# Optimization experiments

Measured on AMD Instinct MI355X. Metric: run time of the kernel, lower is better.

Reference implementation:

```python
import jax, jax.numpy as jnp
import numpy as np

LAMBDA_FGW = 0.5
TAU_KL = 0.1
N_OUTER = 5
N_SINKHORN = 10
DIM = 512


def _pdist(a, b):
    # sqrt(clamp(||a-b||^2, 1e-6)) computed via expansion (avoids BxKxMxD temp)
    n2 = ((a * a).sum(-1)[:, :, None] + (b * b).sum(-1)[:, None, :]
          - 2.0 * jnp.einsum('bkd,bmd->bkm', a, b))
    return jnp.sqrt(jnp.clip(n2, 1e-6, None))


def setup_inputs() -> dict:
    key = jax.random.key(0)
    ks = jax.random.split(key, 10)
    B, K, M, D = 256, 128, 128, DIM
    inp = {
        'sq': jax.random.normal(ks[0], (B, K, D), jnp.float32),
        'sr': jax.random.normal(ks[1], (B, M, D), jnp.float32),
        'mask_q': jax.random.uniform(ks[2], (B, K), jnp.float32),
        'mask_r': jax.random.uniform(ks[3], (B, M), jnp.float32),
        'centroids_q': jax.random.normal(ks[4], (B, K, D), jnp.float32),
        'centroids_r': jax.random.normal(ks[5], (B, M, D), jnp.float32),
        'W1': jax.random.normal(ks[6], (D, D), jnp.float32) * 0.02,
        'b1': jnp.zeros((D,), jnp.float32),
        'W2': jax.random.normal(ks[7], (D, D), jnp.float32) * 0.02,
        'b2': jnp.zeros((D,), jnp.float32),
        'log_eps': jnp.asarray(np.log(0.05), jnp.float32),
    }
    return inp


def reference(sq, sr, mask_q, mask_r, centroids_q, centroids_r, W1, b1, W2, b2, log_eps):
    proj = lambda x: jax.nn.relu(x @ W1 + b1) @ W2 + b2
    pq, pr = proj(sq), proj(sr)
    C = _pdist(pq, pr)                      # [B,K,M]
    Sq = _pdist(centroids_q, centroids_q)   # [B,K,K]
    Sr = _pdist(centroids_r, centroids_r)   # [B,M,M]

    mu = mask_q / (mask_q.sum(-1, keepdims=True) + 1e-8)  # [B,K]
    nu = mask_r / (mask_r.sum(-1, keepdims=True) + 1e-8)  # [B,M]
    T = mu[:, :, None] * nu[:, None, :]

    eps = jnp.clip(jnp.exp(log_eps), 0.01, 0.5)
    rho = TAU_KL / (TAU_KL + eps)
    log_mu = jnp.log(jnp.clip(mu, 1e-8, None))
    log_nu = jnp.log(jnp.clip(nu, 1e-8, None))
    Sq2, Sr2 = Sq * Sq, Sr * Sr

    C_fgw = C
    for _ in range(N_OUTER):
        t1 = jnp.einsum('bkl,bl->bk', Sq2, T.sum(2))[:, :, None]
        t2 = jnp.einsum('bm,bmn->bn', T.sum(1), Sr2)[:, None, :]
        L_gw = t1 + t2 - 2.0 * jnp.einsum('bkl,blm->bkm', Sq, jnp.einsum('blm,bmn->bln', T, Sr))
        C_fgw = (1.0 - LAMBDA_FGW) * C + LAMBDA_FGW * L_gw
        log_K = -C_fgw / eps
        log_u = jnp.zeros_like(mu)
        log_v = jnp.zeros_like(nu)
        for _ in range(N_SINKHORN):
            log_u = rho * (log_mu - jax.nn.logsumexp(log_K + log_v[:, None, :], axis=2))
            log_v = rho * (log_nu - jax.nn.logsumexp(log_K + log_u[:, :, None], axis=1))
        T = jnp.exp(log_u[:, :, None] + log_K + log_v[:, None, :])

    cost = (T * C_fgw).sum((-1, -2))
    similarity = jax.nn.sigmoid(-cost)
    return similarity, T, C, cost
```

## Files before the change

kernel.cpp:

```cpp
#include <hip/hip_runtime.h>
#include <math.h>

typedef unsigned short u16;
typedef __attribute__((ext_vector_type(4))) float f32x4;
typedef __attribute__((ext_vector_type(8))) short bf16x8;
typedef __attribute__((ext_vector_type(4))) unsigned short u16x4;
typedef __attribute__((ext_vector_type(8))) unsigned short u16x8;

#define DEVI static __device__ __forceinline__

DEVI float b2f(u16 u){ union{float f; unsigned i;} v; v.i = ((unsigned)u)<<16; return v.f; }
DEVI u16 f2b(float f){ union{float f; unsigned i;} v; v.f=f;
  unsigned r = v.i + 0x7fffu + ((v.i>>16)&1u); return (u16)(r>>16); }

DEVI void gload_lds16(const void* g, void* l){
  __builtin_amdgcn_global_load_lds((const __attribute__((address_space(1))) void*)g,
                                   (__attribute__((address_space(3))) void*)l, 16, 0, 0);
}

DEVI f32x4 vmax4(f32x4 a, f32x4 b){
  f32x4 r; r[0]=fmaxf(a[0],b[0]); r[1]=fmaxf(a[1],b[1]);
  r[2]=fmaxf(a[2],b[2]); r[3]=fmaxf(a[3],b[3]); return r;
}

__global__ void prepw_k(const float* __restrict__ W, u16* __restrict__ Wt){
  int id = blockIdx.x*256 + threadIdx.x;
  int k = id>>9, c = id&511;
  Wt[c*512 + k] = f2b(W[id]);
}

__global__ void cvt_k(const float* __restrict__ src, u16* __restrict__ dst,
                      float* __restrict__ norms, int nrows){
  int gw = (int)((blockIdx.x*blockDim.x + threadIdx.x)>>6);
  int lane = threadIdx.x & 63;
  if (gw >= nrows) return;
  const float* s = src + (size_t)gw*512;
  u16* d = dst + (size_t)gw*512;
  float acc = 0.f;
  #pragma unroll
  for (int q=0;q<2;q++){
    f32x4 v = *(const f32x4*)(s + q*256 + lane*4);
    u16x4 u;
    #pragma unroll
    for (int e=0;e<4;e++){
      u16 b = f2b(v[e]); u[e] = b;
      float fv = b2f(b); acc += fv*fv;
    }
    *(u16x4*)(d + q*256 + lane*4) = u;
  }
  if (norms != nullptr){
    #pragma unroll
    for (int off=1;off<64;off<<=1) acc += __shfl_xor(acc, off);
    if (lane==0) norms[gw] = acc;
  }
}

template<int ACT, int NORM>
__global__ __launch_bounds__(256) void gemm_k(const u16* __restrict__ X,
    const u16* __restrict__ Wt, const float* __restrict__ bias, u16* __restrict__ OUT,
    float* __restrict__ NP){
  __shared__ __align__(16) u16 sA[128*64];
  __shared__ __align__(16) u16 sB[128*64];
  const int tid = threadIdx.x, wave = tid>>6, lane = tid&63;
  const int bid = (blockIdx.x&7)*256 + (blockIdx.x>>3);
  const int rblk = bid>>2, cb = (bid&3)<<7;
  const u16* Xb = X + (size_t)rblk*(128*512);
  const u16* Wb = Wt + (size_t)cb*512;
  const int lrow = lane&15, lg = lane>>4, wr = wave>>1, wc = wave&1;
  f32x4 acc[4][4] = {};
  for (int s=0;s<8;s++){
    const int k0 = s<<6;
    #pragma unroll
    for (int q=0;q<4;q++){
      const int i = (wave<<2)+q;
      const int row = (i<<3) + (lane>>3);
      const int cd = (lane&7) ^ (row&7);
      gload_lds16(Xb + row*512 + k0 + (cd<<3), sA + i*512);
      gload_lds16(Wb + row*512 + k0 + (cd<<3), sB + i*512);
    }
    __syncthreads();
    #pragma unroll
    for (int kh=0;kh<2;kh++){
      bf16x8 a_[4], b_[4];
      #pragma unroll
      for (int i=0;i<4;i++){
        const int ra = (wr<<6)+(i<<4)+lrow;
        a_[i] = *(const bf16x8*)(sA + ra*64 + ((((kh<<2)+lg)^(ra&7))<<3));
        const int rb = (wc<<6)+(i<<4)+lrow;
        b_[i] = *(const bf16x8*)(sB + rb*64 + ((((kh<<2)+lg)^(rb&7))<<3));
      }
      #pragma unroll
      for (int i=0;i<4;i++)
        #pragma unroll
        for (int j=0;j<4;j++)
          acc[i][j] = __builtin_amdgcn_mfma_f32_16x16x32_bf16(a_[i], b_[j], acc[i][j], 0,0,0);
    }
    __syncthreads();
  }
  float nacc[4][4];
  if (NORM){
    #pragma unroll
    for (int i=0;i<4;i++)
      #pragma unroll
      for (int r=0;r<4;r++) nacc[i][r]=0.f;
  }
  #pragma unroll
  for (int j=0;j<4;j++){
    const int col = cb + (wc<<6) + (j<<4) + lrow;
    const float bv = bias[col];
    #pragma unroll
    for (int i=0;i<4;i++){
      const int row0 = (rblk<<7) + (wr<<6) + (i<<4) + (lg<<2);
      #pragma unroll
      for (int r=0;r<4;r++){
        float v = acc[i][j][r] + bv;
        if (ACT) v = fmaxf(v, 0.f);
        u16 pb = f2b(v);
        OUT[(size_t)(row0+r)*512 + col] = pb;
        if (NORM){ float fv = b2f(pb); nacc[i][r] += fv*fv; }
      }
    }
  }
  if (NORM){
    #pragma unroll
    for (int i=0;i<4;i++)
      #pragma unroll
      for (int r=0;r<4;r++){
        float v = nacc[i][r];
        v += __shfl_xor(v,1); v += __shfl_xor(v,2);
        v += __shfl_xor(v,4); v += __shfl_xor(v,8);
        if (lrow==0)
          atomicAdd(NP + (rblk<<7) + (wr<<6) + (i<<4) + (lg<<2) + r, v);
      }
  }
}

template<int MODE>
__global__ __launch_bounds__(256) void pdist_k(const u16* __restrict__ Xa,
    const u16* __restrict__ Xb2, const float* __restrict__ na, const float* __restrict__ nb,
    float* __restrict__ OUT, char* __restrict__ SHL){
  __shared__ __align__(16) u16 sA[128*64];
  __shared__ __align__(16) u16 sB[128*64];
  const int tid = threadIdx.x, wave = tid>>6, lane = tid&63;
  const int b = blockIdx.x;
  const u16* Ab = Xa + (size_t)b*(128*512);
  const u16* Bb = Xb2 + (size_t)b*(128*512);
  const int lrow = lane&15, lg = lane>>4, wr = wave>>1, wc = wave&1;
  f32x4 acc[4][4] = {};
  for (int s=0;s<8;s++){
    const int k0 = s<<6;
    #pragma unroll
    for (int q=0;q<4;q++){
      const int i = (wave<<2)+q;
      const int row = (i<<3) + (lane>>3);
      const int cd = (lane&7) ^ (row&7);
      gload_lds16(Ab + row*512 + k0 + (cd<<3), sA + i*512);
      gload_lds16(Bb + row*512 + k0 + (cd<<3), sB + i*512);
    }
    __syncthreads();
    #pragma unroll
    for (int kh=0;kh<2;kh++){
      bf16x8 a_[4], b_[4];
      #pragma unroll
      for (int i=0;i<4;i++){
        const int ra = (wr<<6)+(i<<4)+lrow;
        a_[i] = *(const bf16x8*)(sA + ra*64 + ((((kh<<2)+lg)^(ra&7))<<3));
        const int rb = (wc<<6)+(i<<4)+lrow;
        b_[i] = *(const bf16x8*)(sB + rb*64 + ((((kh<<2)+lg)^(rb&7))<<3));
      }
      #pragma unroll
      for (int i=0;i<4;i++)
        #pragma unroll
        for (int j=0;j<4;j++)
          acc[i][j] = __builtin_amdgcn_mfma_f32_16x16x32_bf16(a_[i], b_[j], acc[i][j], 0,0,0);
    }
    __syncthreads();
  }
  #pragma unroll
  for (int j=0;j<4;j++){
    const int col = (wc<<6)+(j<<4)+lrow;
    const float nbv = nb[b*128+col];
    #pragma unroll
    for (int i=0;i<4;i++){
      const int row0 = (wr<<6)+(i<<4)+(lg<<2);
      float sv[4];
      #pragma unroll
      for (int r=0;r<4;r++){
        float n2 = na[b*128+row0+r] + nbv - 2.0f*acc[i][j][r];
        sv[r] = sqrtf(fmaxf(n2, 1e-6f));
      }
      if (MODE==0){
        #pragma unroll
        for (int r=0;r<4;r++)
          OUT[(size_t)b*16384 + (size_t)(row0+r)*128 + col] = sv[r];
      } else {
        u16x4 hi4, lo4;
        #pragma unroll
        for (int r=0;r<4;r++){
          u16 h = f2b(sv[r]); hi4[r] = h;
          lo4[r] = f2b(sv[r] - b2f(h));
        }
        const int sa = col*256 + ((((row0>>3)^col)&15)<<4) + ((row0&7)<<1);
        char* base = SHL + (size_t)b*65536;
        *(u16x4*)(base + sa) = hi4;
        *(u16x4*)(base + 32768 + sa) = lo4;
      }
    }
  }
}

__global__ void prep_k(const float* __restrict__ mask_q, const float* __restrict__ mask_r,
                       float* __restrict__ lmu2, float* __restrict__ lnu2,
                       float* __restrict__ mu, float* __restrict__ nu){
  int b = blockIdx.x, t = threadIdx.x;
  __shared__ float red[4];
  float mq = mask_q[b*128+t], mr = mask_r[b*128+t];
  float s1 = mq, s2 = mr;
  #pragma unroll
  for (int off=1;off<64;off<<=1){ s1 += __shfl_xor(s1,off); s2 += __shfl_xor(s2,off); }
  if ((t&63)==0){ red[t>>6] = s1; red[2+(t>>6)] = s2; }
  __syncthreads();
  float sumq = red[0]+red[1], sumr = red[2]+red[3];
  float muv = mq/(sumq+1e-8f), nuv = mr/(sumr+1e-8f);
  lmu2[b*128+t] = __log2f(fmaxf(muv,1e-8f));
  lnu2[b*128+t] = __log2f(fmaxf(nuv,1e-8f));
  mu[b*128+t] = muv;
  nu[b*128+t] = nuv;
}

__global__ __launch_bounds__(512,1) void fgw_loop_k(
    const char* __restrict__ SQHL, const char* __restrict__ SRHL,
    const float* __restrict__ C_g,
    const float* __restrict__ MU, const float* __restrict__ NU,
    const float* __restrict__ LMU2, const float* __restrict__ LNU2,
    const float* __restrict__ log_eps,
    float* __restrict__ T_out, float* __restrict__ cost_out, float* __restrict__ sim_out)
{
  __shared__ __align__(16) char bufT[65536];
  __shared__ __align__(16) char bufS[65536];
  __shared__ __align__(16) float avs[128], bvs[128], t1s[128], t2s[128];
  __shared__ __align__(16) float lus[128], lvs[128];
  __shared__ float redc[8];

  const int b = blockIdx.x, tid = threadIdx.x;
  const int w = tid>>6, lane = tid&63, l15 = lane&15, lg = lane>>4;
  const char* SqHLb = SQHL + (size_t)b*65536;
  const char* SrHLb = SRHL + (size_t)b*65536;
  const float* Cb   = C_g + (size_t)b*16384;
  const float* MUb  = MU + b*128;
  const float* NUb  = NU + b*128;

  float eps = __expf(log_eps[0]); eps = fminf(fmaxf(eps,0.01f),0.5f);
  const float rho = 0.1f/(0.1f+eps);
  const float hscale = 0.5f*1.4426950408889634f/eps;

  const int kR = 16*w + l15;
  const int n0 = 16*w + 4*lg;
  const float lmu2R = LMU2[b*128+kR];
  const float lnu2C = LNU2[b*128+kR];

  const int rowA256 = (16*w + l15)*256;
  const int glo2 = lg ^ (l15 & 3);
  const int ghi2 = l15 & 12;
  const int wtail = l15*256 + ((((2*w + (lg>>1)) ^ l15)&15)<<4) + ((lg&1)<<3);

  f32x4 Cf2[8];
  #pragma unroll
  for (int kt=0;kt<8;kt++)
    Cf2[kt] = -hscale * (*(const f32x4*)(Cb + (size_t)(16*kt+l15)*128 + n0));

  f32x4 lkR[8], lkC[8];
  float luR = 0.f, lvC = 0.f;

  for (int outer=0; outer<5; outer++){
    #pragma unroll
    for (int r2=0;r2<8;r2++)
      gload_lds16(SrHLb + r2*8192 + tid*16, bufS + r2*8192 + tid*16);
    {
      f32x4 avp = {0.f,0.f,0.f,0.f};
      float bvp = 0.f;
      #pragma unroll
      for (int q=0;q<8;q++){
        f32x4 TR, TC;
        if (outer==0){
          const f32x4 nu4 = *(const f32x4*)(NUb + 16*q + 4*lg);
          const f32x4 mu4 = *(const f32x4*)(MUb + 16*q + 4*lg);
          const float muR = MUb[kR], nuC = NUb[kR];
          TR = muR*nu4; TC = mu4*nuC;
        } else {
          const f32x4 lv4 = *(const f32x4*)&lvs[16*q + 4*lg];
          const f32x4 lu4 = *(const f32x4*)&lus[16*q + 4*lg];
          #pragma unroll
          for (int e=0;e<4;e++){
            TR[e] = exp2f(lkR[q][e] + luR + lv4[e]);
            TC[e] = exp2f(lkC[q][e] + lu4[e] + lvC);
          }
        }
        u16x4 hi4, lo4;
        #pragma unroll
        for (int e=0;e<4;e++){
          u16 h = f2b(TR[e]); hi4[e] = h;
          lo4[e] = f2b(TR[e] - b2f(h));
        }
        const int sa = kR*256 + ((((2*q+(lg>>1)) ^ l15)&15)<<4) + ((lg&1)<<3);
        *(u16x4*)(bufT + sa) = hi4;
        *(u16x4*)(bufT + 32768 + sa) = lo4;
        avp += TR;
        bvp += TC[0]+TC[1]+TC[2]+TC[3];
      }
      float av = avp[0]+avp[1]+avp[2]+avp[3];
      av += __shfl_xor(av,16); av += __shfl_xor(av,32);
      bvp += __shfl_xor(bvp,16); bvp += __shfl_xor(bvp,32);
      if (lg==0){ avs[kR] = av; bvs[kR] = bvp; }
    }
    __syncthreads();

    {
      const int p = tid>>2, sub = tid&3;
      float s2 = 0.f;
      #pragma unroll
      for (int gg=0; gg<4; gg++){
        const int g = 4*sub+gg;
        const int off = p*256 + (((g ^ (p&15))&15)<<4);
        const u16x8 h8 = *(const u16x8*)(bufS + off);
        const u16x8 l8 = *(const u16x8*)(bufS + 32768 + off);
        const f32x4 bva = *(const f32x4*)&bvs[8*g];
        const f32x4 bvb = *(const f32x4*)&bvs[8*g+4];
        #pragma unroll
        for (int e=0;e<4;e++){
          float x = b2f(h8[e]) + b2f(l8[e]);
          s2 = fmaf(bva[e], x*x, s2);
          float y2 = b2f(h8[4+e]) + b2f(l8[4+e]);
          s2 = fmaf(bvb[e], y2*y2, s2);
        }
      }
      s2 += __shfl_xor(s2,1); s2 += __shfl_xor(s2,2);
      if (sub==0) t2s[p] = s2;
    }
    f32x4 acc1[8] = {};
    #pragma unroll
    for (int qt=0;qt<4;qt++){
      const int colOff = (((4*qt) ^ ghi2) | glo2) << 4;
      const bf16x8 ahi = *(const bf16x8*)(bufT + rowA256 + colOff);
      const bf16x8 alo = *(const bf16x8*)(bufT + 32768 + rowA256 + colOff);
      const int bbase = l15*256 + colOff;
      #pragma unroll
      for (int nt=0;nt<8;nt++){
        const bf16x8 bhi = *(const bf16x8*)(bufS + nt*4096 + bbase);
        const bf16x8 blo = *(const bf16x8*)(bufS + 32768 + nt*4096 + bbase);
        acc1[nt] = __builtin_amdgcn_mfma_f32_16x16x32_bf16(ahi, bhi, acc1[nt], 0,0,0);
        acc1[nt] = __builtin_amdgcn_mfma_f32_16x16x32_bf16(ahi, blo, acc1[nt], 0,0,0);
        acc1[nt] = __builtin_amdgcn_mfma_f32_16x16x32_bf16(alo, bhi, acc1[nt], 0,0,0);
      }
    }
    __syncthreads();

    #pragma unroll
    for (int r2=0;r2<8;r2++)
      gload_lds16(SqHLb + r2*8192 + tid*16, bufS + r2*8192 + tid*16);
    #pragma unroll
    for (int nt=0;nt<8;nt++){
      u16x4 hi4, lo4;
      #pragma unroll
      for (int r=0;r<4;r++){
        u16 h = f2b(acc1[nt][r]); hi4[r] = h;
        lo4[r] = f2b(acc1[nt][r] - b2f(h));
      }
      const int sa = nt*4096 + wtail;
      *(u16x4*)(bufT + sa) = hi4;
      *(u16x4*)(bufT + 32768 + sa) = lo4;
    }
    __syncthreads();

    {
      const int p = tid>>2, sub = tid&3;
      float s1 = 0.f;
      #pragma unroll
      for (int gg=0; gg<4; gg++){
        const int g = 4*sub+gg;
        const int off = p*256 + (((g ^ (p&15))&15)<<4);
        const u16x8 h8 = *(const u16x8*)(bufS + off);
        const u16x8 l8 = *(const u16x8*)(bufS + 32768 + off);
        const f32x4 ava = *(const f32x4*)&avs[8*g];
        const f32x4 avb = *(const f32x4*)&avs[8*g+4];
        #pragma unroll
        for (int e=0;e<4;e++){
          float x = b2f(h8[e]) + b2f(l8[e]);
          s1 = fmaf(ava[e], x*x, s1);
          float y2 = b2f(h8[4+e]) + b2f(l8[4+e]);
          s1 = fmaf(avb[e], y2*y2, s1);
        }
      }
      s1 += __shfl_xor(s1,1); s1 += __shfl_xor(s1,2);
      if (sub==0) t1s[p] = s1;
    }
    f32x4 acc2[8] = {};
    #pragma unroll
    for (int qt=0;qt<4;qt++){
      const int colOff = (((4*qt) ^ ghi2) | glo2) << 4;
      const bf16x8 ahi = *(const bf16x8*)(bufT + rowA256 + colOff);
      const bf16x8 alo = *(const bf16x8*)(bufT + 32768 + rowA256 + colOff);
      const int bbase = l15*256 + colOff;
      #pragma unroll
      for (int kt=0;kt<8;kt++){
        const bf16x8 bhi = *(const bf16x8*)(bufS + kt*4096 + bbase);
        const bf16x8 blo = *(const bf16x8*)(bufS + 32768 + kt*4096 + bbase);
        acc2[kt] = __builtin_amdgcn_mfma_f32_16x16x32_bf16(ahi, bhi, acc2[kt], 0,0,0);
        acc2[kt] = __builtin_amdgcn_mfma_f32_16x16x32_bf16(ahi, blo, acc2[kt], 0,0,0);
        acc2[kt] = __builtin_amdgcn_mfma_f32_16x16x32_bf16(alo, bhi, acc2[kt], 0,0,0);
      }
    }
    __syncthreads();

    f32x4 lkf[8];
    {
      const f32x4 t24 = *(const f32x4*)&t2s[n0];
      #pragma unroll
      for (int kt=0;kt<8;kt++){
        const float t1v = t1s[16*kt+l15];
        lkf[kt] = Cf2[kt] + hscale*(2.0f*acc2[kt] - t1v - t24);
      }
    }
    #pragma unroll
    for (int kt=0;kt<8;kt++){
      const int row = 16*kt + l15;
      const int gp = ((4*w+lg) ^ (row&31)) & 31;
      *(f32x4*)(bufT + row*512 + gp*16) = lkf[kt];
      #pragma unroll
      for (int e=0;e<4;e++){
        const int n = n0 + e;
        const int gt = ((4*kt + (l15>>2)) ^ (n&31)) & 31;
        *(float*)(bufS + n*512 + gt*16 + (l15&3)*4) = lkf[kt][e];
      }
    }
    __syncthreads();
    #pragma unroll
    for (int q=0;q<8;q++){
      const int g1 = ((4*q+lg) ^ (kR&31)) & 31;
      lkR[q] = *(const f32x4*)(bufT + kR*512 + g1*16);
      lkC[q] = *(const f32x4*)(bufS + kR*512 + g1*16);
    }

    for (int it=0; it<10; it++){
      f32x4 y[8];
      #pragma unroll
      for (int q=0;q<8;q++){
        y[q] = lkR[q];
        if (it) y[q] += *(const f32x4*)&lvs[16*q+4*lg];
      }
      f32x4 m4 = vmax4(vmax4(vmax4(y[0],y[1]),vmax4(y[2],y[3])),
                       vmax4(vmax4(y[4],y[5]),vmax4(y[6],y[7])));
      float mx = fmaxf(fmaxf(m4[0],m4[1]), fmaxf(m4[2],m4[3]));
      mx = fmaxf(mx,__shfl_xor(mx,16)); mx = fmaxf(mx,__shfl_xor(mx,32));
      f32x4 s4 = {0.f,0.f,0.f,0.f};
      #pragma unroll
      for (int q=0;q<8;q++){
        #pragma unroll
        for (int e=0;e<4;e++) s4[e] += exp2f(y[q][e]-mx);
      }
      float s = s4[0]+s4[1]+s4[2]+s4[3];
      s += __shfl_xor(s,16); s += __shfl_xor(s,32);
      luR = rho*(lmu2R - (mx + __log2f(s)));
      if (lg==0) lus[kR] = luR;
      __syncthreads();
      #pragma unroll
      for (int q=0;q<8;q++)
        y[q] = lkC[q] + *(const f32x4*)&lus[16*q+4*lg];
      m4 = vmax4(vmax4(vmax4(y[0],y[1]),vmax4(y[2],y[3])),
                 vmax4(vmax4(y[4],y[5]),vmax4(y[6],y[7])));
      mx = fmaxf(fmaxf(m4[0],m4[1]), fmaxf(m4[2],m4[3]));
      mx = fmaxf(mx,__shfl_xor(mx,16)); mx = fmaxf(mx,__shfl_xor(mx,32));
      s4 = (f32x4){0.f,0.f,0.f,0.f};
      #pragma unroll
      for (int q=0;q<8;q++){
        #pragma unroll
        for (int e=0;e<4;e++) s4[e] += exp2f(y[q][e]-mx);
      }
      s = s4[0]+s4[1]+s4[2]+s4[3];
      s += __shfl_xor(s,16); s += __shfl_xor(s,32);
      lvC = rho*(lnu2C - (mx + __log2f(s)));
      if (lg==0) lvs[kR] = lvC;
      __syncthreads();
    }

    if (outer==4){
      float cp = 0.f;
      float* Tb = T_out + (size_t)b*16384;
      #pragma unroll
      for (int q=0;q<8;q++){
        const f32x4 lv4 = *(const f32x4*)&lvs[16*q+4*lg];
        f32x4 t;
        #pragma unroll
        for (int e=0;e<4;e++) t[e] = exp2f(lkR[q][e] + luR + lv4[e]);
        *(f32x4*)(Tb + kR*128 + 16*q + 4*lg) = t;
        const f32x4 pr = t*lkR[q];
        cp += pr[0]+pr[1]+pr[2]+pr[3];
      }
      cp *= -eps*0.6931471805599453f;
      #pragma unroll
      for (int off=1;off<64;off<<=1) cp += __shfl_xor(cp, off);
      if (lane==0) redc[w] = cp;
      __syncthreads();
      if (tid==0){
        float tot = 0.f;
        #pragma unroll
        for (int w2=0;w2<8;w2++) tot += redc[w2];
        cost_out[b] = tot;
        sim_out[b]  = 1.0f/(1.0f + __expf(tot));
      }
    }
  }
}

extern "C" void kernel_launch(void* const* d_in, const int* in_sizes, int n_in,
                              void* d_out, int out_size, void* d_ws, size_t ws_size,
                              hipStream_t stream){
  const float* sq      = (const float*)d_in[0];
  const float* sr      = (const float*)d_in[1];
  const float* mask_q  = (const float*)d_in[2];
  const float* mask_r  = (const float*)d_in[3];
  const float* cq      = (const float*)d_in[4];
  const float* cr      = (const float*)d_in[5];
  const float* W1      = (const float*)d_in[6];
  const float* b1      = (const float*)d_in[7];
  const float* W2      = (const float*)d_in[8];
  const float* b2      = (const float*)d_in[9];
  const float* log_eps = (const float*)d_in[10];

  float* out  = (float*)d_out;
  float* sim  = out;
  float* Tm   = out + 256;
  float* Cm   = Tm + 4194304;
  float* cost = Cm + 4194304;

  char* ws = (char*)d_ws;
  size_t off = 0;
  auto alloc = [&](size_t bytes)->void*{ void* p = ws + off; off += (bytes+255)&~(size_t)255; return p; };
  u16*   SQB = (u16*)  alloc(33554432);
  u16*   SRB = (u16*)  alloc(33554432);
  u16*   HQ  = (u16*)  alloc(33554432);
  u16*   HR  = (u16*)  alloc(33554432);
  u16*   W1T = (u16*)  alloc(524288);
  u16*   W2T = (u16*)  alloc(524288);
  float* NP  = (float*)alloc(262144);
  float* NCQ = (float*)alloc(131072);
  float* NCR = (float*)alloc(131072);
  float* LMU = (float*)alloc(131072);
  float* LNU = (float*)alloc(131072);
  float* MUA = (float*)alloc(131072);
  float* NUA = (float*)alloc(131072);
  (void)ws_size; (void)in_sizes; (void)n_in; (void)out_size;

  u16* PQ  = SQB;
  u16* CQB = HQ;
  u16* CRB = HR;

  char* SQHL = (char*)SQB;
  char* SRHL = (char*)SQB + 16777216;

  prepw_k<<<1024,256,0,stream>>>(W1, W1T);
  prepw_k<<<1024,256,0,stream>>>(W2, W2T);
  cvt_k<<<8192,256,0,stream>>>(sq, SQB, nullptr, 32768);
  cvt_k<<<8192,256,0,stream>>>(sr, SRB, nullptr, 32768);
  gemm_k<1,0><<<2048,256,0,stream>>>(SQB, W1T, b1, HQ, nullptr);
  hipMemsetAsync(NP, 0, 262144, stream);
  gemm_k<0,1><<<2048,256,0,stream>>>(HQ, W2T, b2, PQ, NP);
  cvt_k<<<8192,256,0,stream>>>(cq, CQB, NCQ, 32768);
  cvt_k<<<8192,256,0,stream>>>(cr, CRB, NCR, 32768);
  pdist_k<0><<<256,256,0,stream>>>(PQ, PQ + (size_t)32768*512, NP, NP + 32768,
                                   Cm, nullptr);
  pdist_k<1><<<256,256,0,stream>>>(CQB, CQB, NCQ, NCQ, nullptr, SQHL);
  pdist_k<1><<<256,256,0,stream>>>(CRB, CRB, NCR, NCR, nullptr, SRHL);
  prep_k<<<256,128,0,stream>>>(mask_q, mask_r, LMU, LNU, MUA, NUA);
  fgw_loop_k<<<256,512,0,stream>>>(SQHL, SRHL, Cm, MUA, NUA, LMU, LNU,
                                   log_eps, Tm, cost, sim);
}
```

Before: 484.3 us.

## Fuse fp32-to-bf16 conversion into GEMM and self-distance kernels

Drops the separate cvt_k passes. The first projection GEMM now reads fp32 inputs directly and converts them to bf16 while staging into LDS. The centroid self-distance kernel loads fp32 centroids, converts them, computes row norms in-kernel, and uses one shared LDS tile for both operands. This removes four conversion launches and the bf16 intermediate round trips through memory, but the GEMM A-operand load changes from async global-to-LDS to register loads plus LDS stores, which may expose more load latency.

```diff
diff --git a/kernel.cpp b/kernel.cpp
--- a/kernel.cpp
+++ b/kernel.cpp
@@ -29,34 +29,9 @@
   Wt[c*512 + k] = f2b(W[id]);
 }
 
-__global__ void cvt_k(const float* __restrict__ src, u16* __restrict__ dst,
-                      float* __restrict__ norms, int nrows){
-  int gw = (int)((blockIdx.x*blockDim.x + threadIdx.x)>>6);
-  int lane = threadIdx.x & 63;
-  if (gw >= nrows) return;
-  const float* s = src + (size_t)gw*512;
-  u16* d = dst + (size_t)gw*512;
-  float acc = 0.f;
-  #pragma unroll
-  for (int q=0;q<2;q++){
-    f32x4 v = *(const f32x4*)(s + q*256 + lane*4);
-    u16x4 u;
-    #pragma unroll
-    for (int e=0;e<4;e++){
-      u16 b = f2b(v[e]); u[e] = b;
-      float fv = b2f(b); acc += fv*fv;
-    }
-    *(u16x4*)(d + q*256 + lane*4) = u;
-  }
-  if (norms != nullptr){
-    #pragma unroll
-    for (int off=1;off<64;off<<=1) acc += __shfl_xor(acc, off);
-    if (lane==0) norms[gw] = acc;
-  }
-}
-
-template<int ACT, int NORM>
+template<int ACT, int NORM, int AF32>
 __global__ __launch_bounds__(256) void gemm_k(const u16* __restrict__ X,
+    const float* __restrict__ Xf1, const float* __restrict__ Xf2,
     const u16* __restrict__ Wt, const float* __restrict__ bias, u16* __restrict__ OUT,
     float* __restrict__ NP){
   __shared__ __align__(16) u16 sA[128*64];
@@ -64,7 +39,9 @@
   const int tid = threadIdx.x, wave = tid>>6, lane = tid&63;
   const int bid = (blockIdx.x&7)*256 + (blockIdx.x>>3);
   const int rblk = bid>>2, cb = (bid&3)<<7;
-  const u16* Xb = X + (size_t)rblk*(128*512);
+  const u16* Xb = AF32 ? nullptr : (X + (size_t)rblk*(128*512));
+  const float* Xbf = AF32 ? (rblk<256 ? Xf1 + (size_t)rblk*65536
+                                      : Xf2 + (size_t)(rblk-256)*65536) : nullptr;
   const u16* Wb = Wt + (size_t)cb*512;
   const int lrow = lane&15, lg = lane>>4, wr = wave>>1, wc = wave&1;
   f32x4 acc[4][4] = {};
@@ -75,7 +52,17 @@
       const int i = (wave<<2)+q;
       const int row = (i<<3) + (lane>>3);
       const int cd = (lane&7) ^ (row&7);
-      gload_lds16(Xb + row*512 + k0 + (cd<<3), sA + i*512);
+      if (AF32){
+        const float* src = Xbf + row*512 + k0 + (cd<<3);
+        const f32x4 va = *(const f32x4*)src;
+        const f32x4 vb = *(const f32x4*)(src+4);
+        u16x8 t;
+        #pragma unroll
+        for (int e=0;e<4;e++){ t[e]=f2b(va[e]); t[4+e]=f2b(vb[e]); }
+        *(u16x8*)((char*)sA + i*1024 + lane*16) = t;
+      } else {
+        gload_lds16(Xb + row*512 + k0 + (cd<<3), sA + i*512);
+      }
       gload_lds16(Wb + row*512 + k0 + (cd<<3), sB + i*512);
     }
     __syncthreads();
@@ -135,10 +122,9 @@
   }
 }
 
-template<int MODE>
-__global__ __launch_bounds__(256) void pdist_k(const u16* __restrict__ Xa,
+__global__ __launch_bounds__(256) void pdist0_k(const u16* __restrict__ Xa,
     const u16* __restrict__ Xb2, const float* __restrict__ na, const float* __restrict__ nb,
-    float* __restrict__ OUT, char* __restrict__ SHL){
+    float* __restrict__ OUT){
   __shared__ __align__(16) u16 sA[128*64];
   __shared__ __align__(16) u16 sB[128*64];
   const int tid = threadIdx.x, wave = tid>>6, lane = tid&63;
@@ -183,28 +169,87 @@
     #pragma unroll
     for (int i=0;i<4;i++){
       const int row0 = (wr<<6)+(i<<4)+(lg<<2);
-      float sv[4];
       #pragma unroll
       for (int r=0;r<4;r++){
         float n2 = na[b*128+row0+r] + nbv - 2.0f*acc[i][j][r];
-        sv[r] = sqrtf(fmaxf(n2, 1e-6f));
-      }
-      if (MODE==0){
-        #pragma unroll
-        for (int r=0;r<4;r++)
-          OUT[(size_t)b*16384 + (size_t)(row0+r)*128 + col] = sv[r];
-      } else {
-        u16x4 hi4, lo4;
-        #pragma unroll
-        for (int r=0;r<4;r++){
-          u16 h = f2b(sv[r]); hi4[r] = h;
-          lo4[r] = f2b(sv[r] - b2f(h));
-        }
-        const int sa = col*256 + ((((row0>>3)^col)&15)<<4) + ((row0&7)<<1);
-        char* base = SHL + (size_t)b*65536;
-        *(u16x4*)(base + sa) = hi4;
-        *(u16x4*)(base + 32768 + sa) = lo4;
-      }
+        OUT[(size_t)b*16384 + (size_t)(row0+r)*128 + col] = sqrtf(fmaxf(n2, 1e-6f));
+      }
+    }
+  }
+}
+
+__global__ __launch_bounds__(256) void pdistS_k(const float* __restrict__ Sf,
+    char* __restrict__ SHL){
+  __shared__ __align__(16) u16 sA[128*64];
+  __shared__ float nrm[128];
+  const int tid = threadIdx.x, wave = tid>>6, lane = tid&63;
+  const int b = blockIdx.x;
+  const float* Sb = Sf + (size_t)b*65536;
+  const int lrow = lane&15, lg = lane>>4, wr = wave>>1, wc = wave&1;
+  f32x4 acc[4][4] = {};
+  float nacc[4] = {0.f,0.f,0.f,0.f};
+  for (int s=0;s<8;s++){
+    const int k0 = s<<6;
+    #pragma unroll
+    for (int q=0;q<4;q++){
+      const int i = (wave<<2)+q;
+      const int row = (i<<3) + (lane>>3);
+      const int cd = (lane&7) ^ (row&7);
+      const float* src = Sb + row*512 + k0 + (cd<<3);
+      const f32x4 va = *(const f32x4*)src;
+      const f32x4 vb = *(const f32x4*)(src+4);
+      u16x8 t;
+      #pragma unroll
+      for (int e=0;e<4;e++){ t[e]=f2b(va[e]); t[4+e]=f2b(vb[e]); }
+      #pragma unroll
+      for (int e=0;e<8;e++){ float fv=b2f(t[e]); nacc[q]=fmaf(fv,fv,nacc[q]); }
+      *(u16x8*)((char*)sA + i*1024 + lane*16) = t;
+    }
+    __syncthreads();
+    #pragma unroll
+    for (int kh=0;kh<2;kh++){
+      bf16x8 a_[4], b_[4];
+      #pragma unroll
+      for (int i=0;i<4;i++){
+        const int ra = (wr<<6)+(i<<4)+lrow;
+        a_[i] = *(const bf16x8*)(sA + ra*64 + ((((kh<<2)+lg)^(ra&7))<<3));
+        const int rb = (wc<<6)+(i<<4)+lrow;
+        b_[i] = *(const bf16x8*)(sA + rb*64 + ((((kh<<2)+lg)^(rb&7))<<3));
+      }
+      #pragma unroll
+      for (int i=0;i<4;i++)
+        #pragma unroll
+        for (int j=0;j<4;j++)
+          acc[i][j] = __builtin_amdgcn_mfma_f32_16x16x32_bf16(a_[i], b_[j], acc[i][j], 0,0,0);
+    }
+    __syncthreads();
+  }
+  #pragma unroll
+  for (int q=0;q<4;q++){
+    float v = nacc[q];
+    v += __shfl_xor(v,1); v += __shfl_xor(v,2); v += __shfl_xor(v,4);
+    if ((lane&7)==0) nrm[((wave<<2)+q)*8 + (lane>>3)] = v;
+  }
+  __syncthreads();
+  #pragma unroll
+  for (int j=0;j<4;j++){
+    const int col = (wc<<6)+(j<<4)+lrow;
+    const float nbv = nrm[col];
+    #pragma unroll
+    for (int i=0;i<4;i++){
+      const int row0 = (wr<<6)+(i<<4)+(lg<<2);
+      u16x4 hi4, lo4;
+      #pragma unroll
+      for (int r=0;r<4;r++){
+        float n2 = nrm[row0+r] + nbv - 2.0f*acc[i][j][r];
+        float sv = sqrtf(fmaxf(n2, 1e-6f));
+        u16 h = f2b(sv); hi4[r] = h;
+        lo4[r] = f2b(sv - b2f(h));
+      }
+      const int sa = col*256 + ((((row0>>3)^col)&15)<<4) + ((row0&7)<<1);
+      char* base = SHL + (size_t)b*65536;
+      *(u16x4*)(base + sa) = hi4;
+      *(u16x4*)(base + 32768 + sa) = lo4;
     }
   }
 }
@@ -536,41 +581,28 @@
   char* ws = (char*)d_ws;
   size_t off = 0;
   auto alloc = [&](size_t bytes)->void*{ void* p = ws + off; off += (bytes+255)&~(size_t)255; return p; };
-  u16*   SQB = (u16*)  alloc(33554432);
-  u16*   SRB = (u16*)  alloc(33554432);
-  u16*   HQ  = (u16*)  alloc(33554432);
-  u16*   HR  = (u16*)  alloc(33554432);
+  u16*   PQ  = (u16*)  alloc(67108864);
+  u16*   HQ  = (u16*)  alloc(67108864);
   u16*   W1T = (u16*)  alloc(524288);
   u16*   W2T = (u16*)  alloc(524288);
   float* NP  = (float*)alloc(262144);
-  float* NCQ = (float*)alloc(131072);
-  float* NCR = (float*)alloc(131072);
   float* LMU = (float*)alloc(131072);
   float* LNU = (float*)alloc(131072);
   float* MUA = (float*)alloc(131072);
   float* NUA = (float*)alloc(131072);
   (void)ws_size; (void)in_sizes; (void)n_in; (void)out_size;
 
-  u16* PQ  = SQB;
-  u16* CQB = HQ;
-  u16* CRB = HR;
-
-  char* SQHL = (char*)SQB;
-  char* SRHL = (char*)SQB + 16777216;
+  char* SQHL = (char*)PQ;
+  char* SRHL = (char*)PQ + 16777216;
 
   prepw_k<<<1024,256,0,stream>>>(W1, W1T);
   prepw_k<<<1024,256,0,stream>>>(W2, W2T);
-  cvt_k<<<8192,256,0,stream>>>(sq, SQB, nullptr, 32768);
-  cvt_k<<<8192,256,0,stream>>>(sr, SRB, nullptr, 32768);
-  gemm_k<1,0><<<2048,256,0,stream>>>(SQB, W1T, b1, HQ, nullptr);
+  gemm_k<1,0,1><<<2048,256,0,stream>>>(nullptr, sq, sr, W1T, b1, HQ, nullptr);
   hipMemsetAsync(NP, 0, 262144, stream);
-  gemm_k<0,1><<<2048,256,0,stream>>>(HQ, W2T, b2, PQ, NP);
-  cvt_k<<<8192,256,0,stream>>>(cq, CQB, NCQ, 32768);
-  cvt_k<<<8192,256,0,stream>>>(cr, CRB, NCR, 32768);
-  pdist_k<0><<<256,256,0,stream>>>(PQ, PQ + (size_t)32768*512, NP, NP + 32768,
-                                   Cm, nullptr);
-  pdist_k<1><<<256,256,0,stream>>>(CQB, CQB, NCQ, NCQ, nullptr, SQHL);
-  pdist_k<1><<<256,256,0,stream>>>(CRB, CRB, NCR, NCR, nullptr, SRHL);
+  gemm_k<0,1,0><<<2048,256,0,stream>>>(HQ, nullptr, nullptr, W2T, b2, PQ, NP);
+  pdist0_k<<<256,256,0,stream>>>(PQ, PQ + (size_t)32768*512, NP, NP + 32768, Cm);
+  pdistS_k<<<256,256,0,stream>>>(cq, SQHL);
+  pdistS_k<<<256,256,0,stream>>>(cr, SRHL);
   prep_k<<<256,128,0,stream>>>(mask_q, mask_r, LMU, LNU, MUA, NUA);
   fgw_loop_k<<<256,512,0,stream>>>(SQHL, SRHL, Cm, MUA, NUA, LMU, LNU,
                                    log_eps, Tm, cost, sim);
```

Result: faster. 456.6 us (-5.7%).
